# Kernel tuning notes

Hardware: AMD Instinct MI355X
Metric: run time of the kernel (lower is better)

## Reference

```python
import jax, jax.numpy as jnp
import numpy as np

B, L, H, E, V = 64, 2048, 512, 512, 32000


def setup_inputs() -> dict:
    key = jax.random.key(0)
    ks = jax.random.split(key, 12)
    s = 0.02
    return {
        "input_seq": jax.random.randint(ks[0], (B,), 0, V),
        "last_hidden": jax.random.normal(ks[1], (1, B, H), jnp.float32),
        "encoder_outputs": jax.random.normal(ks[2], (B, L, H), jnp.float32),
        "encoder_labels": jax.random.randint(ks[3], (B,), 0, 4),
        "input_feeding_prev_time_step": jnp.zeros((B, H), jnp.float32),
        # learned parameters
        "emb_table": jax.random.normal(ks[4], (V, E), jnp.float32) * s,
        "W_ih": jax.random.normal(ks[5], (3 * H, E), jnp.float32) * s,   # [r|z|n] input weights
        "W_hh": jax.random.normal(ks[6], (3 * H, H), jnp.float32) * s,   # [r|z|n] hidden weights
        "b_ih": jnp.zeros((3 * H,), jnp.float32),
        "b_hh": jnp.zeros((3 * H,), jnp.float32),
        "W_concat": jax.random.normal(ks[7], (H, 2 * H), jnp.float32) * s,
        "b_concat": jnp.zeros((H,), jnp.float32),
        "W_out": jax.random.normal(ks[8], (V, H), jnp.float32) * s,
        "b_out": jnp.zeros((V,), jnp.float32),
    }


def reference(input_seq, last_hidden, encoder_outputs, encoder_labels,
              input_feeding_prev_time_step, emb_table, W_ih, W_hh, b_ih, b_hh,
              W_concat, b_concat, W_out, b_out):
    # embedding lookup (dropout is identity in eval mode)
    x = emb_table[input_seq]                                 # (B, E)
    h = last_hidden[0]                                       # (B, H)
    # single-step GRU cell (PyTorch gate layout: r, z, n)
    gi = x @ W_ih.T + b_ih                                   # (B, 3H)
    gh = h @ W_hh.T + b_hh                                   # (B, 3H)
    i_r, i_z, i_n = jnp.split(gi, 3, axis=-1)
    h_r, h_z, h_n = jnp.split(gh, 3, axis=-1)
    r = jax.nn.sigmoid(i_r + h_r)
    z = jax.nn.sigmoid(i_z + h_z)
    n = jnp.tanh(i_n + r * h_n)
    h_new = (1.0 - z) * n + z * h                            # (B, H)
    # dot attention over encoder outputs
    scores = jnp.einsum("bh,blh->bl", h_new, encoder_outputs)  # (B, L)
    attn = jax.nn.softmax(scores, axis=-1)                   # (B, L)
    context = jnp.einsum("bl,blh->bh", attn, encoder_outputs)  # (B, H)
    # concat -> linear -> tanh -> output projection
    concat_input = jnp.concatenate([h_new, context], axis=-1)  # (B, 2H)
    concat_output = jnp.tanh(concat_input @ W_concat.T + b_concat)  # (B, H)
    output = concat_output @ W_out.T + b_out                 # (B, V)
    last_hidden_state = h_new[None]                          # (1, B, H)
    attn_weights = attn[:, None, :]                          # (B, 1, L)
    return output, last_hidden_state, attn_weights, input_feeding_prev_time_step
```

## Files before the change

### kernel.cpp

```cpp
#include <hip/hip_runtime.h>
#include <hip/hip_bf16.h>
#include <math.h>

#define BB 64
#define LL 2048
#define HH 512
#define EE 512
#define VV 32000
#define H3 1536

typedef __attribute__((ext_vector_type(8))) __bf16 bf16x8;
typedef __attribute__((ext_vector_type(4))) float f32x4;

__device__ __forceinline__ void ld8(const float* __restrict__ p, float* v) {
  float4 a = *(const float4*)p;
  float4 b = *(const float4*)(p + 4);
  v[0]=a.x; v[1]=a.y; v[2]=a.z; v[3]=a.w;
  v[4]=b.x; v[5]=b.y; v[6]=b.z; v[7]=b.w;
}
__device__ __forceinline__ void ld16(const float* __restrict__ p, float* v) {
  ld8(p, v); ld8(p + 8, v + 8);
}
__device__ __forceinline__ float wsum(float v) {
#pragma unroll
  for (int off = 32; off; off >>= 1) v += __shfl_xor(v, off);
  return v;
}
__device__ __forceinline__ unsigned short f2bf(float f) {
  unsigned int u = __float_as_uint(f);
  u = (u + 0x7FFFu + ((u >> 16) & 1u)) >> 16;
  return (unsigned short)u;
}

__global__ __launch_bounds__(256) void k1_gates(
    const int* __restrict__ seq, const float* __restrict__ h,
    const float* __restrict__ emb, const float* __restrict__ Wih,
    const float* __restrict__ Whh, const float* __restrict__ bih,
    const float* __restrict__ bhh, float* __restrict__ gi,
    float* __restrict__ gh) {
  int lane = threadIdx.x & 63;
  int wid = blockIdx.x * 4 + (threadIdx.x >> 6);
  int jp = wid >> 1, bh = wid & 1;
  int j0 = jp * 2;
  float wih[2][8], whh[2][8];
#pragma unroll
  for (int r = 0; r < 2; ++r) {
    ld8(Wih + (size_t)(j0 + r) * EE + lane * 8, wih[r]);
    ld8(Whh + (size_t)(j0 + r) * HH + lane * 8, whh[r]);
  }
  for (int b = bh * 32; b < bh * 32 + 32; ++b) {
    int idx = seq[b];
    float xv[8], hv[8];
    ld8(emb + (size_t)idx * EE + lane * 8, xv);
    ld8(h + b * HH + lane * 8, hv);
#pragma unroll
    for (int r = 0; r < 2; ++r) {
      float di = 0.f, dh = 0.f;
#pragma unroll
      for (int i = 0; i < 8; ++i) {
        di += wih[r][i] * xv[i];
        dh += whh[r][i] * hv[i];
      }
      di = wsum(di);
      dh = wsum(dh);
      if (lane == 0) {
        gi[b * H3 + j0 + r] = di + bih[j0 + r];
        gh[b * H3 + j0 + r] = dh + bhh[j0 + r];
      }
    }
  }
}

__global__ __launch_bounds__(256) void k2_hnew(
    const float* __restrict__ gi, const float* __restrict__ gh,
    const float* __restrict__ h, const float* __restrict__ feed,
    float* __restrict__ cat, float* __restrict__ out1,
    float* __restrict__ out3) {
  int t = blockIdx.x * 256 + threadIdx.x;
  int b = t >> 9, k = t & 511;
  const float* gib = gi + b * H3;
  const float* ghb = gh + b * H3;
  float r = 1.f / (1.f + __expf(-(gib[k] + ghb[k])));
  float z = 1.f / (1.f + __expf(-(gib[k + HH] + ghb[k + HH])));
  float n = tanhf(gib[k + 2 * HH] + r * ghb[k + 2 * HH]);
  float hn = (1.f - z) * n + z * h[t];
  cat[b * 1024 + k] = hn;
  out1[t] = hn;
  out3[t] = feed[t];
}

__global__ __launch_bounds__(256) void k3_attn(
    const float* __restrict__ enc, const float* __restrict__ cat,
    float* __restrict__ scores, float* __restrict__ pm,
    float* __restrict__ ps, float* __restrict__ pc) {
  int b = blockIdx.y, ch = blockIdx.x;
  int w = threadIdx.x >> 6, lane = threadIdx.x & 63;
  float hv[8];
  ld8(cat + b * 1024 + lane * 8, hv);
  float m = -INFINITY, s = 0.f, c[8];
#pragma unroll
  for (int j = 0; j < 8; ++j) c[j] = 0.f;
  const float* eb = enc + ((size_t)b * LL + ch * 128) * HH;
  for (int i = 0; i < 32; ++i) {
    int l = w + i * 4;
    float ev[8];
    ld8(eb + (size_t)l * HH + lane * 8, ev);
    float d = 0.f;
#pragma unroll
    for (int j = 0; j < 8; ++j) d += hv[j] * ev[j];
    d = wsum(d);
    if (lane == 0) scores[b * LL + ch * 128 + l] = d;
    if (d > m) {
      float sc = __expf(m - d);
      s *= sc;
#pragma unroll
      for (int j = 0; j < 8; ++j) c[j] *= sc;
      m = d;
    }
    float wgt = __expf(d - m);
    s += wgt;
#pragma unroll
    for (int j = 0; j < 8; ++j) c[j] += wgt * ev[j];
  }
  __shared__ float sm[4], ssum[4];
  __shared__ float scx[4][512];
  if (lane == 0) { sm[w] = m; ssum[w] = s; }
#pragma unroll
  for (int j = 0; j < 8; ++j) scx[w][lane * 8 + j] = c[j];
  __syncthreads();
  float mb = fmaxf(fmaxf(sm[0], sm[1]), fmaxf(sm[2], sm[3]));
  int t = threadIdx.x;
  if (t == 0) {
    float sb = 0.f;
#pragma unroll
    for (int w2 = 0; w2 < 4; ++w2) sb += ssum[w2] * __expf(sm[w2] - mb);
    pm[b * 16 + ch] = mb;
    ps[b * 16 + ch] = sb;
  }
  for (int k = t; k < 512; k += 256) {
    float v = 0.f;
#pragma unroll
    for (int w2 = 0; w2 < 4; ++w2) v += scx[w2][k] * __expf(sm[w2] - mb);
    pc[(size_t)(b * 16 + ch) * 512 + k] = v;
  }
}

__global__ __launch_bounds__(512) void k4_ctx(
    const float* __restrict__ pm, const float* __restrict__ ps,
    const float* __restrict__ pc, float* __restrict__ cat,
    float* __restrict__ mden) {
  int b = blockIdx.x;
  int k = threadIdx.x;
  float mb = -INFINITY;
#pragma unroll
  for (int ch = 0; ch < 16; ++ch) mb = fmaxf(mb, pm[b * 16 + ch]);
  float den = 0.f, v = 0.f;
#pragma unroll
  for (int ch = 0; ch < 16; ++ch) {
    float e = __expf(pm[b * 16 + ch] - mb);
    den += ps[b * 16 + ch] * e;
    v += pc[(size_t)(b * 16 + ch) * 512 + k] * e;
  }
  cat[b * 1024 + 512 + k] = v / den;
  if (k == 0) { mden[b * 2] = mb; mden[b * 2 + 1] = den; }
}

__global__ __launch_bounds__(256) void k5_attnw(
    const float* __restrict__ scores, const float* __restrict__ mden,
    float* __restrict__ out2) {
  int t = blockIdx.x * 256 + threadIdx.x;
  int b = t >> 11;
  out2[t] = __expf(scores[t] - mden[b * 2]) / mden[b * 2 + 1];
}

__global__ __launch_bounds__(256) void k6_concat(
    const float* __restrict__ cat, const float* __restrict__ Wc,
    const float* __restrict__ bc, unsigned short* __restrict__ co_bf) {
  int lane = threadIdx.x & 63;
  int wid = blockIdx.x * 4 + (threadIdx.x >> 6);
  int k = wid >> 3, bg = wid & 7;
  float wv[16];
  ld16(Wc + (size_t)k * 1024 + lane * 16, wv);
  float bk = bc[k];
  for (int b = bg * 8; b < bg * 8 + 8; ++b) {
    float cv[16];
    ld16(cat + b * 1024 + lane * 16, cv);
    float d = 0.f;
#pragma unroll
    for (int i = 0; i < 16; ++i) d += wv[i] * cv[i];
    d = wsum(d);
    if (lane == 0) co_bf[b * HH + k] = f2bf(tanhf(d + bk));
  }
}

__global__ __launch_bounds__(256) void k7_out(
    const unsigned short* __restrict__ co_bf, const float* __restrict__ Wo,
    const float* __restrict__ bo, float* __restrict__ out0) {
  int t = threadIdx.x;
  int lane = t & 63, w = t >> 6;
  int v0 = blockIdx.x * 64 + w * 16;
  int l15 = lane & 15;
  int kbase = (lane >> 4) * 8;
  int vrow = v0 + l15;
  const float* wrow = Wo + (size_t)vrow * HH;

  f32x4 acc[4];
#pragma unroll
  for (int j = 0; j < 4; ++j) acc[j] = (f32x4){0.f, 0.f, 0.f, 0.f};

  for (int ks = 0; ks < HH; ks += 32) {
    int k = ks + kbase;
    float4 wa = *(const float4*)(wrow + k);
    float4 wb = *(const float4*)(wrow + k + 4);
    union { unsigned short u[8]; bf16x8 v; } B;
    B.u[0] = f2bf(wa.x); B.u[1] = f2bf(wa.y);
    B.u[2] = f2bf(wa.z); B.u[3] = f2bf(wa.w);
    B.u[4] = f2bf(wb.x); B.u[5] = f2bf(wb.y);
    B.u[6] = f2bf(wb.z); B.u[7] = f2bf(wb.w);
#pragma unroll
    for (int j = 0; j < 4; ++j) {
      bf16x8 A = *(const bf16x8*)(co_bf + (size_t)(j * 16 + l15) * HH + k);
      acc[j] = __builtin_amdgcn_mfma_f32_16x16x32_bf16(A, B.v, acc[j], 0, 0, 0);
    }
  }

  float bias = bo[vrow];
#pragma unroll
  for (int j = 0; j < 4; ++j) {
    int b0 = j * 16 + (lane >> 4) * 4;
#pragma unroll
    for (int r = 0; r < 4; ++r) {
      out0[(size_t)(b0 + r) * VV + vrow] = acc[j][r] + bias;
    }
  }
}

extern "C" void kernel_launch(void* const* d_in, const int* in_sizes, int n_in,
                              void* d_out, int out_size, void* d_ws,
                              size_t ws_size, hipStream_t stream) {
  const int* seq = (const int*)d_in[0];
  const float* last_hidden = (const float*)d_in[1];
  const float* enc = (const float*)d_in[2];
  const float* feed = (const float*)d_in[4];
  const float* emb = (const float*)d_in[5];
  const float* Wih = (const float*)d_in[6];
  const float* Whh = (const float*)d_in[7];
  const float* bih = (const float*)d_in[8];
  const float* bhh = (const float*)d_in[9];
  const float* Wc = (const float*)d_in[10];
  const float* bc = (const float*)d_in[11];
  const float* Wo = (const float*)d_in[12];
  const float* bo = (const float*)d_in[13];

  float* out = (float*)d_out;
  float* out0 = out;
  float* out1 = out + 2048000;
  float* out2 = out + 2080768;
  float* out3 = out + 2211840;

  float* ws = (float*)d_ws;
  float* gi = ws;
  float* gh = gi + 98304;
  float* cat = gh + 98304;
  float* scores = cat + 65536;
  float* pm = scores + 131072;
  float* ps = pm + 1024;
  float* pc = ps + 1024;
  float* mden = pc + 524288;
  unsigned short* co_bf = (unsigned short*)(mden + 128);

  hipLaunchKernelGGL(k1_gates, dim3(384), dim3(256), 0, stream,
                     seq, last_hidden, emb, Wih, Whh, bih, bhh, gi, gh);
  hipLaunchKernelGGL(k2_hnew, dim3(128), dim3(256), 0, stream,
                     gi, gh, last_hidden, feed, cat, out1, out3);
  hipLaunchKernelGGL(k3_attn, dim3(16, 64), dim3(256), 0, stream,
                     enc, cat, scores, pm, ps, pc);
  hipLaunchKernelGGL(k4_ctx, dim3(64), dim3(512), 0, stream,
                     pm, ps, pc, cat, mden);
  hipLaunchKernelGGL(k5_attnw, dim3(512), dim3(256), 0, stream,
                     scores, mden, out2);
  hipLaunchKernelGGL(k6_concat, dim3(1024), dim3(256), 0, stream,
                     cat, Wc, bc, co_bf);
  hipLaunchKernelGGL(k7_out, dim3(500), dim3(256), 0, stream,
                     co_bf, Wo, bo, out0);
}
```

Measured before the change: 133.5 us.

## Fuse GRU finalize into attention kernel, merge context and softmax kernels, batch enc loads

Every attention block now recomputes the GRU hidden update from gi/gh itself, and only one wave writes h_new, the feed copy and the concat slot, so the separate k2 launch goes away. The attention loop issues four encoder row loads per iteration and updates the online softmax max once per group, which raises memory-level parallelism. The context reduction and the attention-weight normalisation are merged into one kernel, removing two more launches and the mden buffer. The cost is redundant gate math in all 16 chunk blocks and more registers in k3.

```diff
diff --git a/kernel.cpp b/kernel.cpp
--- a/kernel.cpp
+++ b/kernel.cpp
@@ -71,62 +71,88 @@
   }
 }
 
-__global__ __launch_bounds__(256) void k2_hnew(
-    const float* __restrict__ gi, const float* __restrict__ gh,
-    const float* __restrict__ h, const float* __restrict__ feed,
-    float* __restrict__ cat, float* __restrict__ out1,
-    float* __restrict__ out3) {
-  int t = blockIdx.x * 256 + threadIdx.x;
-  int b = t >> 9, k = t & 511;
-  const float* gib = gi + b * H3;
-  const float* ghb = gh + b * H3;
-  float r = 1.f / (1.f + __expf(-(gib[k] + ghb[k])));
-  float z = 1.f / (1.f + __expf(-(gib[k + HH] + ghb[k + HH])));
-  float n = tanhf(gib[k + 2 * HH] + r * ghb[k + 2 * HH]);
-  float hn = (1.f - z) * n + z * h[t];
-  cat[b * 1024 + k] = hn;
-  out1[t] = hn;
-  out3[t] = feed[t];
-}
-
 __global__ __launch_bounds__(256) void k3_attn(
-    const float* __restrict__ enc, const float* __restrict__ cat,
+    const float* __restrict__ enc, const float* __restrict__ gi,
+    const float* __restrict__ gh, const float* __restrict__ h,
+    const float* __restrict__ feed, float* __restrict__ cat,
+    float* __restrict__ out1, float* __restrict__ out3,
     float* __restrict__ scores, float* __restrict__ pm,
     float* __restrict__ ps, float* __restrict__ pc) {
   int b = blockIdx.y, ch = blockIdx.x;
   int w = threadIdx.x >> 6, lane = threadIdx.x & 63;
+  int k0 = lane * 8;
+
   float hv[8];
-  ld8(cat + b * 1024 + lane * 8, hv);
+  {
+    float gr[8], gz[8], gn[8], hr[8], hz[8], hn_[8], hh[8];
+    const float* gib = gi + b * H3;
+    const float* ghb = gh + b * H3;
+    ld8(gib + k0, gr); ld8(gib + 512 + k0, gz); ld8(gib + 1024 + k0, gn);
+    ld8(ghb + k0, hr); ld8(ghb + 512 + k0, hz); ld8(ghb + 1024 + k0, hn_);
+    ld8(h + b * HH + k0, hh);
+#pragma unroll
+    for (int i = 0; i < 8; ++i) {
+      float r = 1.f / (1.f + __expf(-(gr[i] + hr[i])));
+      float z = 1.f / (1.f + __expf(-(gz[i] + hz[i])));
+      float n = tanhf(gn[i] + r * hn_[i]);
+      hv[i] = (1.f - z) * n + z * hh[i];
+    }
+    if (ch == 0 && w == 0) {
+      float fv[8];
+      ld8(feed + b * HH + k0, fv);
+#pragma unroll
+      for (int i = 0; i < 8; ++i) {
+        out1[b * HH + k0 + i] = hv[i];
+        cat[b * 1024 + k0 + i] = hv[i];
+        out3[b * HH + k0 + i] = fv[i];
+      }
+    }
+  }
+
   float m = -INFINITY, s = 0.f, c[8];
 #pragma unroll
   for (int j = 0; j < 8; ++j) c[j] = 0.f;
   const float* eb = enc + ((size_t)b * LL + ch * 128) * HH;
-  for (int i = 0; i < 32; ++i) {
-    int l = w + i * 4;
-    float ev[8];
-    ld8(eb + (size_t)l * HH + lane * 8, ev);
-    float d = 0.f;
-#pragma unroll
-    for (int j = 0; j < 8; ++j) d += hv[j] * ev[j];
-    d = wsum(d);
-    if (lane == 0) scores[b * LL + ch * 128 + l] = d;
-    if (d > m) {
-      float sc = __expf(m - d);
+  for (int it = 0; it < 8; ++it) {
+    float ev[4][8], d[4];
+#pragma unroll
+    for (int q = 0; q < 4; ++q) {
+      int l = w + (it * 4 + q) * 4;
+      ld8(eb + (size_t)l * HH + k0, ev[q]);
+    }
+#pragma unroll
+    for (int q = 0; q < 4; ++q) {
+      float dd = 0.f;
+#pragma unroll
+      for (int j = 0; j < 8; ++j) dd += hv[j] * ev[q][j];
+      d[q] = wsum(dd);
+    }
+    if (lane == 0) {
+#pragma unroll
+      for (int q = 0; q < 4; ++q)
+        scores[b * LL + ch * 128 + w + (it * 4 + q) * 4] = d[q];
+    }
+    float g = fmaxf(fmaxf(d[0], d[1]), fmaxf(d[2], d[3]));
+    if (g > m) {
+      float sc = __expf(m - g);
       s *= sc;
 #pragma unroll
       for (int j = 0; j < 8; ++j) c[j] *= sc;
-      m = d;
-    }
-    float wgt = __expf(d - m);
-    s += wgt;
-#pragma unroll
-    for (int j = 0; j < 8; ++j) c[j] += wgt * ev[j];
+      m = g;
+    }
+#pragma unroll
+    for (int q = 0; q < 4; ++q) {
+      float wq = __expf(d[q] - m);
+      s += wq;
+#pragma unroll
+      for (int j = 0; j < 8; ++j) c[j] += wq * ev[q][j];
+    }
   }
   __shared__ float sm[4], ssum[4];
   __shared__ float scx[4][512];
   if (lane == 0) { sm[w] = m; ssum[w] = s; }
 #pragma unroll
-  for (int j = 0; j < 8; ++j) scx[w][lane * 8 + j] = c[j];
+  for (int j = 0; j < 8; ++j) scx[w][k0 + j] = c[j];
   __syncthreads();
   float mb = fmaxf(fmaxf(sm[0], sm[1]), fmaxf(sm[2], sm[3]));
   int t = threadIdx.x;
@@ -145,32 +171,33 @@
   }
 }
 
-__global__ __launch_bounds__(512) void k4_ctx(
+__global__ __launch_bounds__(256) void k45_ctx(
     const float* __restrict__ pm, const float* __restrict__ ps,
-    const float* __restrict__ pc, float* __restrict__ cat,
-    float* __restrict__ mden) {
+    const float* __restrict__ pc, const float* __restrict__ scores,
+    float* __restrict__ cat, float* __restrict__ out2) {
   int b = blockIdx.x;
-  int k = threadIdx.x;
+  int tid = threadIdx.x;
   float mb = -INFINITY;
 #pragma unroll
   for (int ch = 0; ch < 16; ++ch) mb = fmaxf(mb, pm[b * 16 + ch]);
-  float den = 0.f, v = 0.f;
+  float e[16];
+  float den = 0.f;
 #pragma unroll
   for (int ch = 0; ch < 16; ++ch) {
-    float e = __expf(pm[b * 16 + ch] - mb);
-    den += ps[b * 16 + ch] * e;
-    v += pc[(size_t)(b * 16 + ch) * 512 + k] * e;
-  }
-  cat[b * 1024 + 512 + k] = v / den;
-  if (k == 0) { mden[b * 2] = mb; mden[b * 2 + 1] = den; }
-}
-
-__global__ __launch_bounds__(256) void k5_attnw(
-    const float* __restrict__ scores, const float* __restrict__ mden,
-    float* __restrict__ out2) {
-  int t = blockIdx.x * 256 + threadIdx.x;
-  int b = t >> 11;
-  out2[t] = __expf(scores[t] - mden[b * 2]) / mden[b * 2 + 1];
+    e[ch] = __expf(pm[b * 16 + ch] - mb);
+    den += ps[b * 16 + ch] * e[ch];
+  }
+  for (int k = tid; k < 512; k += 256) {
+    float v = 0.f;
+#pragma unroll
+    for (int ch = 0; ch < 16; ++ch)
+      v += pc[(size_t)(b * 16 + ch) * 512 + k] * e[ch];
+    cat[b * 1024 + 512 + k] = v / den;
+  }
+  float inv = 1.f / den;
+  for (int t = tid; t < LL; t += 256) {
+    out2[b * LL + t] = __expf(scores[b * LL + t] - mb) * inv;
+  }
 }
 
 __global__ __launch_bounds__(256) void k6_concat(
@@ -266,19 +293,15 @@
   float* pm = scores + 131072;
   float* ps = pm + 1024;
   float* pc = ps + 1024;
-  float* mden = pc + 524288;
-  unsigned short* co_bf = (unsigned short*)(mden + 128);
+  unsigned short* co_bf = (unsigned short*)(pc + 524288);
 
   hipLaunchKernelGGL(k1_gates, dim3(384), dim3(256), 0, stream,
                      seq, last_hidden, emb, Wih, Whh, bih, bhh, gi, gh);
-  hipLaunchKernelGGL(k2_hnew, dim3(128), dim3(256), 0, stream,
-                     gi, gh, last_hidden, feed, cat, out1, out3);
   hipLaunchKernelGGL(k3_attn, dim3(16, 64), dim3(256), 0, stream,
-                     enc, cat, scores, pm, ps, pc);
-  hipLaunchKernelGGL(k4_ctx, dim3(64), dim3(512), 0, stream,
-                     pm, ps, pc, cat, mden);
-  hipLaunchKernelGGL(k5_attnw, dim3(512), dim3(256), 0, stream,
-                     scores, mden, out2);
+                     enc, gi, gh, last_hidden, feed, cat, out1, out3,
+                     scores, pm, ps, pc);
+  hipLaunchKernelGGL(k45_ctx, dim3(64), dim3(256), 0, stream,
+                     pm, ps, pc, scores, cat, out2);
   hipLaunchKernelGGL(k6_concat, dim3(1024), dim3(256), 0, stream,
                      cat, Wc, bc, co_bf);
   hipLaunchKernelGGL(k7_out, dim3(500), dim3(256), 0, stream,
```

Measured after the change: 135.7 us. No clear change (+1.7%).

## Stage encoder chunks in LDS, split attention finer, fuse context and softmax-weight kernels

Applied to the files above, without the earlier changes.

The attention kernel now splits each batch row into 64 chunks of 32 rows instead of 16 chunks of 128. Each block copies its chunk of encoder outputs into shared memory with wide batched loads, then runs a branchless online softmax over the staged rows. The context reduction and attention-weight normalisation are merged into one kernel, and the gate kernel double-buffers its embedding and hidden-state loads. In exchange, partial-context workspace and the reduction loop in the merged kernel grow fourfold, and the merged kernel runs only 64 blocks.

```diff
diff --git a/kernel.cpp b/kernel.cpp
--- a/kernel.cpp
+++ b/kernel.cpp
@@ -8,6 +8,8 @@
 #define EE 512
 #define VV 32000
 #define H3 1536
+#define CH_ROWS 32
+#define NCH 64
 
 typedef __attribute__((ext_vector_type(8))) __bf16 bf16x8;
 typedef __attribute__((ext_vector_type(4))) float f32x4;
@@ -30,6 +32,28 @@
   unsigned int u = __float_as_uint(f);
   u = (u + 0x7FFFu + ((u >> 16) & 1u)) >> 16;
   return (unsigned short)u;
+}
+
+__device__ __forceinline__ void k1_proc(
+    const float wih[2][8], const float whh[2][8], const float xv[8],
+    const float hv[8], int b, int j0, int lane,
+    const float* __restrict__ bih, const float* __restrict__ bhh,
+    float* __restrict__ gi, float* __restrict__ gh) {
+#pragma unroll
+  for (int r = 0; r < 2; ++r) {
+    float di = 0.f, dh = 0.f;
+#pragma unroll
+    for (int i = 0; i < 8; ++i) {
+      di += wih[r][i] * xv[i];
+      dh += whh[r][i] * hv[i];
+    }
+    di = wsum(di);
+    dh = wsum(dh);
+    if (lane == 0) {
+      gi[b * H3 + j0 + r] = di + bih[j0 + r];
+      gh[b * H3 + j0 + r] = dh + bhh[j0 + r];
+    }
+  }
 }
 
 __global__ __launch_bounds__(256) void k1_gates(
@@ -48,26 +72,21 @@
     ld8(Wih + (size_t)(j0 + r) * EE + lane * 8, wih[r]);
     ld8(Whh + (size_t)(j0 + r) * HH + lane * 8, whh[r]);
   }
-  for (int b = bh * 32; b < bh * 32 + 32; ++b) {
-    int idx = seq[b];
-    float xv[8], hv[8];
-    ld8(emb + (size_t)idx * EE + lane * 8, xv);
-    ld8(h + b * HH + lane * 8, hv);
-#pragma unroll
-    for (int r = 0; r < 2; ++r) {
-      float di = 0.f, dh = 0.f;
-#pragma unroll
-      for (int i = 0; i < 8; ++i) {
-        di += wih[r][i] * xv[i];
-        dh += whh[r][i] * hv[i];
-      }
-      di = wsum(di);
-      dh = wsum(dh);
-      if (lane == 0) {
-        gi[b * H3 + j0 + r] = di + bih[j0 + r];
-        gh[b * H3 + j0 + r] = dh + bhh[j0 + r];
-      }
-    }
+  int bs = bh * 32;
+  float xvA[8], hvA[8], xvB[8], hvB[8];
+  ld8(emb + (size_t)seq[bs] * EE + lane * 8, xvA);
+  ld8(h + bs * HH + lane * 8, hvA);
+#pragma unroll
+  for (int bi = 0; bi < 32; bi += 2) {
+    int b = bs + bi;
+    ld8(emb + (size_t)seq[b + 1] * EE + lane * 8, xvB);
+    ld8(h + (b + 1) * HH + lane * 8, hvB);
+    k1_proc(wih, whh, xvA, hvA, b, j0, lane, bih, bhh, gi, gh);
+    if (bi + 2 < 32) {
+      ld8(emb + (size_t)seq[b + 2] * EE + lane * 8, xvA);
+      ld8(h + (b + 2) * HH + lane * 8, hvA);
+    }
+    k1_proc(wih, whh, xvB, hvB, b + 1, j0, lane, bih, bhh, gi, gh);
   }
 }
 
@@ -93,84 +112,107 @@
     const float* __restrict__ enc, const float* __restrict__ cat,
     float* __restrict__ scores, float* __restrict__ pm,
     float* __restrict__ ps, float* __restrict__ pc) {
+  __shared__ float lds[CH_ROWS * HH];
   int b = blockIdx.y, ch = blockIdx.x;
-  int w = threadIdx.x >> 6, lane = threadIdx.x & 63;
-  float hv[8];
-  ld8(cat + b * 1024 + lane * 8, hv);
-  float m = -INFINITY, s = 0.f, c[8];
-#pragma unroll
-  for (int j = 0; j < 8; ++j) c[j] = 0.f;
-  const float* eb = enc + ((size_t)b * LL + ch * 128) * HH;
-  for (int i = 0; i < 32; ++i) {
-    int l = w + i * 4;
-    float ev[8];
-    ld8(eb + (size_t)l * HH + lane * 8, ev);
-    float d = 0.f;
-#pragma unroll
-    for (int j = 0; j < 8; ++j) d += hv[j] * ev[j];
+  int tid = threadIdx.x, w = tid >> 6, lane = tid & 63;
+
+  const float* eb = enc + ((size_t)b * LL + ch * CH_ROWS) * HH;
+  float4 h4a = *(const float4*)(cat + b * 1024 + 4 * lane);
+  float4 h4b = *(const float4*)(cat + b * 1024 + 256 + 4 * lane);
+
+  {
+    const float4* src = (const float4*)eb;
+    float4* dst = (float4*)lds;
+    float4 buf[8];
+#pragma unroll
+    for (int i = 0; i < 8; ++i) buf[i] = src[tid + 256 * i];
+#pragma unroll
+    for (int i = 0; i < 8; ++i) dst[tid + 256 * i] = buf[i];
+#pragma unroll
+    for (int i = 0; i < 8; ++i) buf[i] = src[tid + 256 * (i + 8)];
+#pragma unroll
+    for (int i = 0; i < 8; ++i) dst[tid + 256 * (i + 8)] = buf[i];
+  }
+  __syncthreads();
+
+  float m = -INFINITY, s = 0.f;
+  float4 ca = {0.f, 0.f, 0.f, 0.f}, cb = {0.f, 0.f, 0.f, 0.f};
+  float* srow = scores + b * LL + ch * CH_ROWS;
+#pragma unroll
+  for (int j = 0; j < 8; ++j) {
+    int r = w + 4 * j;
+    float4 ea = *(const float4*)&lds[r * HH + 4 * lane];
+    float4 e2 = *(const float4*)&lds[r * HH + 256 + 4 * lane];
+    float d = ea.x * h4a.x + ea.y * h4a.y + ea.z * h4a.z + ea.w * h4a.w +
+              e2.x * h4b.x + e2.y * h4b.y + e2.z * h4b.z + e2.w * h4b.w;
     d = wsum(d);
-    if (lane == 0) scores[b * LL + ch * 128 + l] = d;
-    if (d > m) {
-      float sc = __expf(m - d);
-      s *= sc;
-#pragma unroll
-      for (int j = 0; j < 8; ++j) c[j] *= sc;
-      m = d;
-    }
-    float wgt = __expf(d - m);
-    s += wgt;
-#pragma unroll
-    for (int j = 0; j < 8; ++j) c[j] += wgt * ev[j];
-  }
-  __shared__ float sm[4], ssum[4];
-  __shared__ float scx[4][512];
+    if (lane == 0) srow[r] = d;
+    float mn = fmaxf(m, d);
+    float sc = __expf(m - mn);
+    float wq = __expf(d - mn);
+    s = s * sc + wq;
+    ca.x = ca.x * sc + wq * ea.x;
+    ca.y = ca.y * sc + wq * ea.y;
+    ca.z = ca.z * sc + wq * ea.z;
+    ca.w = ca.w * sc + wq * ea.w;
+    cb.x = cb.x * sc + wq * e2.x;
+    cb.y = cb.y * sc + wq * e2.y;
+    cb.z = cb.z * sc + wq * e2.z;
+    cb.w = cb.w * sc + wq * e2.w;
+    m = mn;
+  }
+  __syncthreads();
+
+  float* sm = lds;
+  float* ssum = lds + 4;
+  float* scx = lds + 8;
   if (lane == 0) { sm[w] = m; ssum[w] = s; }
-#pragma unroll
-  for (int j = 0; j < 8; ++j) scx[w][lane * 8 + j] = c[j];
+  ((float4*)(scx + w * 512))[lane] = ca;
+  ((float4*)(scx + w * 512 + 256))[lane] = cb;
   __syncthreads();
   float mb = fmaxf(fmaxf(sm[0], sm[1]), fmaxf(sm[2], sm[3]));
-  int t = threadIdx.x;
-  if (t == 0) {
+  if (tid == 0) {
     float sb = 0.f;
 #pragma unroll
     for (int w2 = 0; w2 < 4; ++w2) sb += ssum[w2] * __expf(sm[w2] - mb);
-    pm[b * 16 + ch] = mb;
-    ps[b * 16 + ch] = sb;
-  }
-  for (int k = t; k < 512; k += 256) {
+    pm[b * NCH + ch] = mb;
+    ps[b * NCH + ch] = sb;
+  }
+  for (int k = tid; k < 512; k += 256) {
     float v = 0.f;
 #pragma unroll
-    for (int w2 = 0; w2 < 4; ++w2) v += scx[w2][k] * __expf(sm[w2] - mb);
-    pc[(size_t)(b * 16 + ch) * 512 + k] = v;
-  }
-}
-
-__global__ __launch_bounds__(512) void k4_ctx(
+    for (int w2 = 0; w2 < 4; ++w2) v += scx[w2 * 512 + k] * __expf(sm[w2] - mb);
+    pc[(size_t)(b * NCH + ch) * 512 + k] = v;
+  }
+}
+
+__global__ __launch_bounds__(256) void k45_ctx(
     const float* __restrict__ pm, const float* __restrict__ ps,
-    const float* __restrict__ pc, float* __restrict__ cat,
-    float* __restrict__ mden) {
+    const float* __restrict__ pc, const float* __restrict__ scores,
+    float* __restrict__ cat, float* __restrict__ out2) {
   int b = blockIdx.x;
-  int k = threadIdx.x;
+  int tid = threadIdx.x;
   float mb = -INFINITY;
 #pragma unroll
-  for (int ch = 0; ch < 16; ++ch) mb = fmaxf(mb, pm[b * 16 + ch]);
-  float den = 0.f, v = 0.f;
-#pragma unroll
-  for (int ch = 0; ch < 16; ++ch) {
-    float e = __expf(pm[b * 16 + ch] - mb);
-    den += ps[b * 16 + ch] * e;
-    v += pc[(size_t)(b * 16 + ch) * 512 + k] * e;
-  }
-  cat[b * 1024 + 512 + k] = v / den;
-  if (k == 0) { mden[b * 2] = mb; mden[b * 2 + 1] = den; }
-}
-
-__global__ __launch_bounds__(256) void k5_attnw(
-    const float* __restrict__ scores, const float* __restrict__ mden,
-    float* __restrict__ out2) {
-  int t = blockIdx.x * 256 + threadIdx.x;
-  int b = t >> 11;
-  out2[t] = __expf(scores[t] - mden[b * 2]) / mden[b * 2 + 1];
+  for (int ch = 0; ch < NCH; ++ch) mb = fmaxf(mb, pm[b * NCH + ch]);
+  float e[NCH];
+  float den = 0.f;
+#pragma unroll
+  for (int ch = 0; ch < NCH; ++ch) {
+    e[ch] = __expf(pm[b * NCH + ch] - mb);
+    den += ps[b * NCH + ch] * e[ch];
+  }
+  for (int k = tid; k < 512; k += 256) {
+    float v = 0.f;
+#pragma unroll
+    for (int ch = 0; ch < NCH; ++ch)
+      v += pc[(size_t)(b * NCH + ch) * 512 + k] * e[ch];
+    cat[b * 1024 + 512 + k] = v / den;
+  }
+  float inv = 1.f / den;
+  for (int t = tid; t < LL; t += 256) {
+    out2[b * LL + t] = __expf(scores[b * LL + t] - mb) * inv;
+  }
 }
 
 __global__ __launch_bounds__(256) void k6_concat(
@@ -264,21 +306,18 @@
   float* cat = gh + 98304;
   float* scores = cat + 65536;
   float* pm = scores + 131072;
-  float* ps = pm + 1024;
-  float* pc = ps + 1024;
-  float* mden = pc + 524288;
-  unsigned short* co_bf = (unsigned short*)(mden + 128);
+  float* ps = pm + 4096;
+  float* pc = ps + 4096;
+  unsigned short* co_bf = (unsigned short*)(pc + 2097152);
 
   hipLaunchKernelGGL(k1_gates, dim3(384), dim3(256), 0, stream,
                      seq, last_hidden, emb, Wih, Whh, bih, bhh, gi, gh);
   hipLaunchKernelGGL(k2_hnew, dim3(128), dim3(256), 0, stream,
                      gi, gh, last_hidden, feed, cat, out1, out3);
-  hipLaunchKernelGGL(k3_attn, dim3(16, 64), dim3(256), 0, stream,
+  hipLaunchKernelGGL(k3_attn, dim3(NCH, BB), dim3(256), 0, stream,
                      enc, cat, scores, pm, ps, pc);
-  hipLaunchKernelGGL(k4_ctx, dim3(64), dim3(512), 0, stream,
-                     pm, ps, pc, cat, mden);
-  hipLaunchKernelGGL(k5_attnw, dim3(512), dim3(256), 0, stream,
-                     scores, mden, out2);
+  hipLaunchKernelGGL(k45_ctx, dim3(64), dim3(256), 0, stream,
+                     pm, ps, pc, scores, cat, out2);
   hipLaunchKernelGGL(k6_concat, dim3(1024), dim3(256), 0, stream,
                      cat, Wc, bc, co_bf);
   hipLaunchKernelGGL(k7_out, dim3(500), dim3(256), 0, stream,
```

Measured after the change: 160.8 us. 1.2x slower.
